# Optimization experiments

Hardware: AMD Instinct MI355X
Metric: run time of the kernel (lower is better)

Reference implementation:

```python
import jax, jax.numpy as jnp
import numpy as np

DIM = 256
HEADS = 8
QUERY_IDX = 0


def setup_inputs() -> dict:
    key = jax.random.key(0)
    ks = jax.random.split(key, 9)
    B, N, D = 32, 8192, DIM
    s = 0.02
    return {
        "x": jax.random.normal(ks[0], (B, N, D), dtype=jnp.float32),
        "Wq": jax.random.normal(ks[1], (D, D), dtype=jnp.float32) * s,
        "bq": jnp.zeros((D,), dtype=jnp.float32),
        "Wk": jax.random.normal(ks[2], (D, D), dtype=jnp.float32) * s,
        "bk": jnp.zeros((D,), dtype=jnp.float32),
        "Wv": jax.random.normal(ks[3], (D, D), dtype=jnp.float32) * s,
        "bv": jnp.zeros((D,), dtype=jnp.float32),
        "Wo": jax.random.normal(ks[4], (D, D), dtype=jnp.float32) * s,
        "bo": jnp.zeros((D,), dtype=jnp.float32),
    }


def reference(x, Wq, bq, Wk, bk, Wv, bv, Wo, bo):
    B, N, D = x.shape
    H = HEADS
    dh = D // H
    scale = 1.0 / np.sqrt(dh)
    # single-token query slice [B, 1, D]
    q = jax.lax.dynamic_slice_in_dim(x, QUERY_IDX, 1, axis=1)
    Q = (q @ Wq + bq).reshape(B, 1, H, dh)
    K = (x @ Wk + bk).reshape(B, N, H, dh)
    V = (x @ Wv + bv).reshape(B, N, H, dh)
    # decode-style attention: one query vs N keys per head
    scores = jnp.einsum("bqhd,bkhd->bhqk", Q, K) * scale  # [B,H,1,N]
    w = jax.nn.softmax(scores, axis=-1)
    attn = jnp.einsum("bhqk,bkhd->bqhd", w, V).reshape(B, 1, D)
    residual = attn @ Wo + bo
    return q + residual
```

## Files before the change

kernel.cpp:

```cpp
#include <hip/hip_runtime.h>


namespace {
constexpr int DIMC = 256;
constexpr int NHEAD = 8;
constexpr int NTOKENS = 8192;
constexpr int NBATCH = 32;
constexpr int TOK_PER_BLOCK = 128;
constexpr int CHUNKS = NTOKENS / TOK_PER_BLOCK;
constexpr float SCALE = 0.17677669529663687f;

constexpr int WS_SCTX = 0;
constexpr int WS_L    = NBATCH * NHEAD * DIMC;
constexpr int WS_QK   = WS_L + NBATCH * NHEAD;
constexpr int WS_QB   = WS_QK + NBATCH * NHEAD * DIMC;
constexpr int WS_PART = WS_QB + NBATCH * NHEAD;
constexpr size_t WS_NEEDED_BYTES =
    (size_t)(WS_PART + NBATCH * CHUNKS * NHEAD * DIMC) * 4;
}

template <int CTRL>
__device__ __forceinline__ float dppmov(float v) {
  return __int_as_float(
      __builtin_amdgcn_update_dpp(0, __float_as_int(v), CTRL, 0xF, 0xF, true));
}
template <int PAT>
__device__ __forceinline__ float swzf(float v) {
  return __int_as_float(__builtin_amdgcn_ds_swizzle(__float_as_int(v), PAT));
}

__global__ __launch_bounds__(256) void k1_prep(
    const float* __restrict__ x, const float* __restrict__ Wq,
    const float* __restrict__ bq, const float* __restrict__ Wk,
    const float* __restrict__ bk, float* __restrict__ qk_g,
    float* __restrict__ qb_g, float* __restrict__ sctx_g,
    float* __restrict__ l_g) {
  const int b = blockIdx.x, tid = threadIdx.x;
  __shared__ float xs[DIMC];
  __shared__ float Qs[DIMC];
  __shared__ float wk[DIMC][33];
  xs[tid] = x[(size_t)b * NTOKENS * DIMC + tid];
#pragma unroll
  for (int r = 0; r < NHEAD; ++r) sctx_g[b * NHEAD * DIMC + r * DIMC + tid] = 0.f;
  if (tid < NHEAD) l_g[b * NHEAD + tid] = 0.f;
  __syncthreads();
  {
    float a0 = bq[tid], a1 = 0.f, a2 = 0.f, a3 = 0.f;
#pragma unroll 8
    for (int d = 0; d < DIMC; d += 4) {
      a0 += xs[d + 0] * Wq[(d + 0) * DIMC + tid];
      a1 += xs[d + 1] * Wq[(d + 1) * DIMC + tid];
      a2 += xs[d + 2] * Wq[(d + 2) * DIMC + tid];
      a3 += xs[d + 3] * Wq[(d + 3) * DIMC + tid];
    }
    Qs[tid] = (a0 + a1) + (a2 + a3);
  }
  __syncthreads();
  for (int h = 0; h < NHEAD; ++h) {
#pragma unroll
    for (int kk = 0; kk < 32; ++kk) {
      const int i = kk * 256 + tid;
      wk[i >> 5][i & 31] = Wk[(size_t)(i >> 5) * DIMC + h * 32 + (i & 31)];
    }
    __syncthreads();
    float s0 = 0.f, s1 = 0.f, s2 = 0.f, s3 = 0.f;
#pragma unroll
    for (int j = 0; j < 32; j += 4) {
      s0 += Qs[h * 32 + j + 0] * wk[tid][j + 0];
      s1 += Qs[h * 32 + j + 1] * wk[tid][j + 1];
      s2 += Qs[h * 32 + j + 2] * wk[tid][j + 2];
      s3 += Qs[h * 32 + j + 3] * wk[tid][j + 3];
    }
    qk_g[b * NHEAD * DIMC + h * DIMC + tid] = SCALE * ((s0 + s1) + (s2 + s3));
    __syncthreads();
  }
  if (tid < NHEAD) {
    float s = 0.f;
#pragma unroll
    for (int j = 0; j < 32; ++j) s += Qs[tid * 32 + j] * bk[tid * 32 + j];
    qb_g[b * NHEAD + tid] = SCALE * s;
  }
}

template <bool PARTIAL>
__global__ __launch_bounds__(256) void k2_attn(
    const float* __restrict__ x, const float* __restrict__ qk_g,
    const float* __restrict__ qb_g, float* __restrict__ dst_g,
    float* __restrict__ l_g) {
  const int b = blockIdx.x >> 6;
  const int chunk = blockIdx.x & (CHUNKS - 1);
  const int tid = threadIdx.x;
  const int wave = tid >> 6;
  const int lane = tid & 63;
  const int q2 = lane & 3;
  const bool c0 = (lane & 1) != 0, c1 = (lane & 2) != 0;

  const float4* qkp = (const float4*)(qk_g + b * NHEAD * DIMC);
  float4 qk[8];
#pragma unroll
  for (int h = 0; h < 8; ++h) qk[h] = qkp[h * 64 + lane];
  const float qba = qb_g[b * 8 + q2];
  const float qbb = qb_g[b * 8 + 4 + q2];

  float4 sc[8];
#pragma unroll
  for (int j = 0; j < 8; ++j) sc[j] = make_float4(0.f, 0.f, 0.f, 0.f);
  float laccA = 0.f, laccB = 0.f;

  const int n0 = chunk * TOK_PER_BLOCK + wave * 32;
  const float4* xp = (const float4*)(x + (size_t)b * NTOKENS * DIMC);

  float4 xa[8], xb[8];
#pragma unroll
  for (int u = 0; u < 8; ++u) xa[u] = xp[(size_t)(n0 + u) * 64 + lane];

#pragma unroll 1
  for (int g = 0; g < 4; ++g) {
    if (g < 3) {
      const int n1 = n0 + (g + 1) * 8;
#pragma unroll
      for (int u = 0; u < 8; ++u) xb[u] = xp[(size_t)(n1 + u) * 64 + lane];
    }
    float va[8], vb[8];
#pragma unroll
    for (int u = 0; u < 8; ++u) {
      float p[8];
#pragma unroll
      for (int h = 0; h < 8; ++h)
        p[h] = xa[u].x * qk[h].x + xa[u].y * qk[h].y + xa[u].z * qk[h].z +
               xa[u].w * qk[h].w;
#pragma unroll
      for (int h = 0; h < 8; ++h) {
        p[h] += dppmov<0xB1>(p[h]);
        p[h] += dppmov<0x4E>(p[h]);
      }
      float t0 = c0 ? p[1] : p[0], t1 = c0 ? p[3] : p[2];
      float s0 = c0 ? p[5] : p[4], s1 = c0 ? p[7] : p[6];
      va[u] = c1 ? t1 : t0;
      vb[u] = c1 ? s1 : s0;
    }
#pragma unroll
    for (int u = 0; u < 8; ++u) { va[u] += swzf<0x101F>(va[u]); vb[u] += swzf<0x101F>(vb[u]); }
#pragma unroll
    for (int u = 0; u < 8; ++u) { va[u] += dppmov<0x128>(va[u]); vb[u] += dppmov<0x128>(vb[u]); }
#pragma unroll
    for (int u = 0; u < 8; ++u) { va[u] += swzf<0x401F>(va[u]); vb[u] += swzf<0x401F>(vb[u]); }
#pragma unroll
    for (int u = 0; u < 8; ++u) { va[u] += __shfl_xor(va[u], 32, 64); vb[u] += __shfl_xor(vb[u], 32, 64); }
    float ea[8], eb[8];
#pragma unroll
    for (int u = 0; u < 8; ++u) {
      ea[u] = __expf(va[u] + qba);
      eb[u] = __expf(vb[u] + qbb);
      laccA += ea[u];
      laccB += eb[u];
    }
#pragma unroll
    for (int u = 0; u < 8; ++u) {
      float r0 = ea[u], r1 = dppmov<0xB1>(ea[u]);
      float r2 = dppmov<0x4E>(ea[u]), r3 = dppmov<0x4E>(r1);
      float r4 = eb[u], r5 = dppmov<0xB1>(eb[u]);
      float r6 = dppmov<0x4E>(eb[u]), r7 = dppmov<0x4E>(r5);
      sc[0].x += r0 * xa[u].x; sc[0].y += r0 * xa[u].y; sc[0].z += r0 * xa[u].z; sc[0].w += r0 * xa[u].w;
      sc[1].x += r1 * xa[u].x; sc[1].y += r1 * xa[u].y; sc[1].z += r1 * xa[u].z; sc[1].w += r1 * xa[u].w;
      sc[2].x += r2 * xa[u].x; sc[2].y += r2 * xa[u].y; sc[2].z += r2 * xa[u].z; sc[2].w += r2 * xa[u].w;
      sc[3].x += r3 * xa[u].x; sc[3].y += r3 * xa[u].y; sc[3].z += r3 * xa[u].z; sc[3].w += r3 * xa[u].w;
      sc[4].x += r4 * xa[u].x; sc[4].y += r4 * xa[u].y; sc[4].z += r4 * xa[u].z; sc[4].w += r4 * xa[u].w;
      sc[5].x += r5 * xa[u].x; sc[5].y += r5 * xa[u].y; sc[5].z += r5 * xa[u].z; sc[5].w += r5 * xa[u].w;
      sc[6].x += r6 * xa[u].x; sc[6].y += r6 * xa[u].y; sc[6].z += r6 * xa[u].z; sc[6].w += r6 * xa[u].w;
      sc[7].x += r7 * xa[u].x; sc[7].y += r7 * xa[u].y; sc[7].z += r7 * xa[u].z; sc[7].w += r7 * xa[u].w;
    }
    if (g < 3) {
#pragma unroll
      for (int u = 0; u < 8; ++u) xa[u] = xb[u];
    }
  }

  if constexpr (PARTIAL) {
    __shared__ float4 red[2][8][64];
    if (wave >= 2) {
#pragma unroll
      for (int j = 0; j < 8; ++j) red[wave - 2][j][lane] = sc[j];
    }
    __syncthreads();
    if (wave < 2) {
#pragma unroll
      for (int j = 0; j < 8; ++j) {
        float4 v = red[wave][j][lane];
        sc[j].x += v.x; sc[j].y += v.y; sc[j].z += v.z; sc[j].w += v.w;
      }
    }
    __syncthreads();
    if (wave == 1) {
#pragma unroll
      for (int j = 0; j < 8; ++j) red[0][j][lane] = sc[j];
    }
    __syncthreads();
    if (wave == 0) {
      float4* pp = (float4*)dst_g + ((size_t)(b * CHUNKS + chunk) * 8) * 64 + lane;
#pragma unroll
      for (int j = 0; j < 8; ++j) {
        float4 v = red[0][j][lane];
        sc[j].x += v.x; sc[j].y += v.y; sc[j].z += v.z; sc[j].w += v.w;
        pp[j * 64] = sc[j];
      }
    }
  } else {
    float* sb = dst_g + b * NHEAD * DIMC;
    const int dbase = lane * 4;
#pragma unroll
    for (int j = 0; j < 8; ++j) {
      const int h = (j < 4) ? (q2 ^ j) : (4 + (q2 ^ (j - 4)));
      atomicAdd(&sb[h * DIMC + dbase + 0], sc[j].x);
      atomicAdd(&sb[h * DIMC + dbase + 1], sc[j].y);
      atomicAdd(&sb[h * DIMC + dbase + 2], sc[j].z);
      atomicAdd(&sb[h * DIMC + dbase + 3], sc[j].w);
    }
  }

  if (lane < 4) {
    atomicAdd(&l_g[b * 8 + lane], laccA);
    atomicAdd(&l_g[b * 8 + 4 + lane], laccB);
  }
}

template <bool FROMPART>
__global__ __launch_bounds__(256) void k3_final(
    const float* __restrict__ x, const float* __restrict__ Wv,
    const float* __restrict__ bv, const float* __restrict__ Wo,
    const float* __restrict__ bo, const float* __restrict__ src,
    const float* __restrict__ l_g, float* __restrict__ out) {
  const int b = blockIdx.x, tid = threadIdx.x;
  __shared__ float ctxs[NHEAD * 260];
  __shared__ float os[DIMC];
  __shared__ float ls[NHEAD];
  if (tid < NHEAD) ls[tid] = l_g[b * NHEAD + tid];
  if constexpr (FROMPART) {
    const int lane = tid & 63, j = tid >> 6, q2 = lane & 3;
    const float4* p0 =
        (const float4*)src + ((size_t)(b * CHUNKS) * 8 + j) * 64 + lane;
    float4 a0 = make_float4(0.f, 0.f, 0.f, 0.f);
    float4 a1 = make_float4(0.f, 0.f, 0.f, 0.f);
    for (int c = 0; c < CHUNKS; ++c) {
      float4 v0 = p0[(size_t)c * 512];
      float4 v1 = p0[(size_t)c * 512 + 256];
      a0.x += v0.x; a0.y += v0.y; a0.z += v0.z; a0.w += v0.w;
      a1.x += v1.x; a1.y += v1.y; a1.z += v1.z; a1.w += v1.w;
    }
    const int h0 = q2 ^ j, h1 = 4 + (q2 ^ j);
    *(float4*)&ctxs[h0 * 260 + lane * 4] = a0;
    *(float4*)&ctxs[h1 * 260 + lane * 4] = a1;
  } else {
#pragma unroll
    for (int r = 0; r < NHEAD; ++r)
      ctxs[r * 260 + tid] = src[b * NHEAD * DIMC + r * DIMC + tid];
  }
  __syncthreads();
  const int h = tid >> 5;
  {
    float s0 = 0.f, s1 = 0.f, s2 = 0.f, s3 = 0.f;
#pragma unroll 8
    for (int d = 0; d < DIMC; d += 4) {
      s0 += ctxs[h * 260 + d + 0] * Wv[(d + 0) * DIMC + tid];
      s1 += ctxs[h * 260 + d + 1] * Wv[(d + 1) * DIMC + tid];
      s2 += ctxs[h * 260 + d + 2] * Wv[(d + 2) * DIMC + tid];
      s3 += ctxs[h * 260 + d + 3] * Wv[(d + 3) * DIMC + tid];
    }
    os[tid] = ((s0 + s1) + (s2 + s3)) / ls[h] + bv[tid];
  }
  __syncthreads();
  {
    float a0 = bo[tid] + x[(size_t)b * NTOKENS * DIMC + tid];
    float a1 = 0.f, a2 = 0.f, a3 = 0.f;
#pragma unroll 8
    for (int j = 0; j < DIMC; j += 4) {
      a0 += os[j + 0] * Wo[(j + 0) * DIMC + tid];
      a1 += os[j + 1] * Wo[(j + 1) * DIMC + tid];
      a2 += os[j + 2] * Wo[(j + 2) * DIMC + tid];
      a3 += os[j + 3] * Wo[(j + 3) * DIMC + tid];
    }
    out[b * DIMC + tid] = (a0 + a1) + (a2 + a3);
  }
}

extern "C" void kernel_launch(void* const* d_in, const int* in_sizes, int n_in,
                              void* d_out, int out_size, void* d_ws, size_t ws_size,
                              hipStream_t stream) {
  const float* x  = (const float*)d_in[0];
  const float* Wq = (const float*)d_in[1];
  const float* bq = (const float*)d_in[2];
  const float* Wk = (const float*)d_in[3];
  const float* bk = (const float*)d_in[4];
  const float* Wv = (const float*)d_in[5];
  const float* bv = (const float*)d_in[6];
  const float* Wo = (const float*)d_in[7];
  const float* bo = (const float*)d_in[8];
  float* ws = (float*)d_ws;
  float* sctx = ws + WS_SCTX;
  float* lg   = ws + WS_L;
  float* qk   = ws + WS_QK;
  float* qb   = ws + WS_QB;
  float* part = ws + WS_PART;

  k1_prep<<<NBATCH, 256, 0, stream>>>(x, Wq, bq, Wk, bk, qk, qb, sctx, lg);
  if (ws_size >= WS_NEEDED_BYTES) {
    k2_attn<true><<<NBATCH * CHUNKS, 256, 0, stream>>>(x, qk, qb, part, lg);
    k3_final<true><<<NBATCH, 256, 0, stream>>>(x, Wv, bv, Wo, bo, part, lg,
                                               (float*)d_out);
  } else {
    k2_attn<false><<<NBATCH * CHUNKS, 256, 0, stream>>>(x, qk, qb, sctx, lg);
    k3_final<false><<<NBATCH, 256, 0, stream>>>(x, Wv, bv, Wo, bo, sctx, lg,
                                                (float*)d_out);
  }
}
```

Before: 455.9 us.

## Double tokens per block, shrink prefetch depth, and use transpose-reduce with permlane swaps

Each block now covers 256 tokens (64 per wave) with a 4-token double buffer instead of 8, which halves the number of blocks and the partial results to merge. The per-token head reduction becomes a transpose-style butterfly: pairs of heads are combined with DPP, then row reductions use DPP row_shr and the gfx950 permlane16/32 swap builtins instead of ds_swizzle and cross-lane shuffles through LDS. The aim is to cut reduction instruction count and LDS-routed permutes, and to lower register pressure. The cost is less memory-level parallelism per wave and fewer blocks for the GPU to spread across its units.

```diff
diff --git a/kernel.cpp b/kernel.cpp
--- a/kernel.cpp
+++ b/kernel.cpp
@@ -6,7 +6,7 @@
 constexpr int NHEAD = 8;
 constexpr int NTOKENS = 8192;
 constexpr int NBATCH = 32;
-constexpr int TOK_PER_BLOCK = 128;
+constexpr int TOK_PER_BLOCK = 256;
 constexpr int CHUNKS = NTOKENS / TOK_PER_BLOCK;
 constexpr float SCALE = 0.17677669529663687f;
 
@@ -27,6 +27,25 @@
 template <int PAT>
 __device__ __forceinline__ float swzf(float v) {
   return __int_as_float(__builtin_amdgcn_ds_swizzle(__float_as_int(v), PAT));
+}
+
+__device__ __forceinline__ float sum_x16(float v) {
+#if __has_builtin(__builtin_amdgcn_permlane16_swap)
+  auto r = __builtin_amdgcn_permlane16_swap(__float_as_int(v), __float_as_int(v),
+                                            false, false);
+  return __int_as_float(r[0]) + __int_as_float(r[1]);
+#else
+  return v + swzf<0x401F>(v);
+#endif
+}
+__device__ __forceinline__ float sum_x32(float v) {
+#if __has_builtin(__builtin_amdgcn_permlane32_swap)
+  auto r = __builtin_amdgcn_permlane32_swap(__float_as_int(v), __float_as_int(v),
+                                            false, false);
+  return __int_as_float(r[0]) + __int_as_float(r[1]);
+#else
+  return v + __shfl_xor(v, 32, 64);
+#endif
 }
 
 __global__ __launch_bounds__(256) void k1_prep(
@@ -87,7 +106,7 @@
     const float* __restrict__ x, const float* __restrict__ qk_g,
     const float* __restrict__ qb_g, float* __restrict__ dst_g,
     float* __restrict__ l_g) {
-  const int b = blockIdx.x >> 6;
+  const int b = blockIdx.x >> 5;
   const int chunk = blockIdx.x & (CHUNKS - 1);
   const int tid = threadIdx.x;
   const int wave = tid >> 6;
@@ -107,60 +126,46 @@
   for (int j = 0; j < 8; ++j) sc[j] = make_float4(0.f, 0.f, 0.f, 0.f);
   float laccA = 0.f, laccB = 0.f;
 
-  const int n0 = chunk * TOK_PER_BLOCK + wave * 32;
+  const int n0 = chunk * TOK_PER_BLOCK + wave * 64;
   const float4* xp = (const float4*)(x + (size_t)b * NTOKENS * DIMC);
 
-  float4 xa[8], xb[8];
-#pragma unroll
-  for (int u = 0; u < 8; ++u) xa[u] = xp[(size_t)(n0 + u) * 64 + lane];
+  float4 xa[4], xb[4];
+#pragma unroll
+  for (int u = 0; u < 4; ++u) xa[u] = xp[(size_t)(n0 + u) * 64 + lane];
 
 #pragma unroll 1
-  for (int g = 0; g < 4; ++g) {
-    if (g < 3) {
-      const int n1 = n0 + (g + 1) * 8;
-#pragma unroll
-      for (int u = 0; u < 8; ++u) xb[u] = xp[(size_t)(n1 + u) * 64 + lane];
-    }
-    float va[8], vb[8];
-#pragma unroll
-    for (int u = 0; u < 8; ++u) {
+  for (int g = 0; g < 16; ++g) {
+    if (g < 15) {
+      const int n1 = n0 + (g + 1) * 4;
+#pragma unroll
+      for (int u = 0; u < 4; ++u) xb[u] = xp[(size_t)(n1 + u) * 64 + lane];
+    }
+#pragma unroll
+    for (int u = 0; u < 4; ++u) {
       float p[8];
 #pragma unroll
       for (int h = 0; h < 8; ++h)
         p[h] = xa[u].x * qk[h].x + xa[u].y * qk[h].y + xa[u].z * qk[h].z +
                xa[u].w * qk[h].w;
-#pragma unroll
-      for (int h = 0; h < 8; ++h) {
-        p[h] += dppmov<0xB1>(p[h]);
-        p[h] += dppmov<0x4E>(p[h]);
-      }
-      float t0 = c0 ? p[1] : p[0], t1 = c0 ? p[3] : p[2];
-      float s0 = c0 ? p[5] : p[4], s1 = c0 ? p[7] : p[6];
-      va[u] = c1 ? t1 : t0;
-      vb[u] = c1 ? s1 : s0;
-    }
-#pragma unroll
-    for (int u = 0; u < 8; ++u) { va[u] += swzf<0x101F>(va[u]); vb[u] += swzf<0x101F>(vb[u]); }
-#pragma unroll
-    for (int u = 0; u < 8; ++u) { va[u] += dppmov<0x128>(va[u]); vb[u] += dppmov<0x128>(vb[u]); }
-#pragma unroll
-    for (int u = 0; u < 8; ++u) { va[u] += swzf<0x401F>(va[u]); vb[u] += swzf<0x401F>(vb[u]); }
-#pragma unroll
-    for (int u = 0; u < 8; ++u) { va[u] += __shfl_xor(va[u], 32, 64); vb[u] += __shfl_xor(vb[u], 32, 64); }
-    float ea[8], eb[8];
-#pragma unroll
-    for (int u = 0; u < 8; ++u) {
-      ea[u] = __expf(va[u] + qba);
-      eb[u] = __expf(vb[u] + qbb);
-      laccA += ea[u];
-      laccB += eb[u];
-    }
-#pragma unroll
-    for (int u = 0; u < 8; ++u) {
-      float r0 = ea[u], r1 = dppmov<0xB1>(ea[u]);
-      float r2 = dppmov<0x4E>(ea[u]), r3 = dppmov<0x4E>(r1);
-      float r4 = eb[u], r5 = dppmov<0xB1>(eb[u]);
-      float r6 = dppmov<0x4E>(eb[u]), r7 = dppmov<0x4E>(r5);
+      float q01 = (c0 ? p[1] : p[0]) + dppmov<0xB1>(c0 ? p[0] : p[1]);
+      float q23 = (c0 ? p[3] : p[2]) + dppmov<0xB1>(c0 ? p[2] : p[3]);
+      float q45 = (c0 ? p[5] : p[4]) + dppmov<0xB1>(c0 ? p[4] : p[5]);
+      float q67 = (c0 ? p[7] : p[6]) + dppmov<0xB1>(c0 ? p[6] : p[7]);
+      float va = (c1 ? q23 : q01) + dppmov<0x4E>(c1 ? q01 : q23);
+      float vb = (c1 ? q67 : q45) + dppmov<0x4E>(c1 ? q45 : q67);
+      va += dppmov<0x124>(va); vb += dppmov<0x124>(vb);
+      va += dppmov<0x128>(va); vb += dppmov<0x128>(vb);
+      va = sum_x16(va); vb = sum_x16(vb);
+      va = sum_x32(va); vb = sum_x32(vb);
+
+      const float ea = __expf(va + qba);
+      const float eb = __expf(vb + qbb);
+      laccA += ea; laccB += eb;
+
+      float r0 = ea, r1 = dppmov<0xB1>(ea);
+      float r2 = dppmov<0x4E>(ea), r3 = dppmov<0x4E>(r1);
+      float r4 = eb, r5 = dppmov<0xB1>(eb);
+      float r6 = dppmov<0x4E>(eb), r7 = dppmov<0x4E>(r5);
       sc[0].x += r0 * xa[u].x; sc[0].y += r0 * xa[u].y; sc[0].z += r0 * xa[u].z; sc[0].w += r0 * xa[u].w;
       sc[1].x += r1 * xa[u].x; sc[1].y += r1 * xa[u].y; sc[1].z += r1 * xa[u].z; sc[1].w += r1 * xa[u].w;
       sc[2].x += r2 * xa[u].x; sc[2].y += r2 * xa[u].y; sc[2].z += r2 * xa[u].z; sc[2].w += r2 * xa[u].w;
@@ -170,9 +175,9 @@
       sc[6].x += r6 * xa[u].x; sc[6].y += r6 * xa[u].y; sc[6].z += r6 * xa[u].z; sc[6].w += r6 * xa[u].w;
       sc[7].x += r7 * xa[u].x; sc[7].y += r7 * xa[u].y; sc[7].z += r7 * xa[u].z; sc[7].w += r7 * xa[u].w;
     }
-    if (g < 3) {
-#pragma unroll
-      for (int u = 0; u < 8; ++u) xa[u] = xb[u];
+    if (g < 15) {
+#pragma unroll
+      for (int u = 0; u < 4; ++u) xa[u] = xb[u];
     }
   }
 
```

New measurement: 419.4 us. 8.0% less time.
